# Kernel optimization log

Measured on AMD Instinct MI355X. Metric: run time of the kernel, lower is better.

The kernel has to match this reference:

```python
import jax, jax.numpy as jnp
import numpy as np

NUM_HEAVY = 1024
N_ITERS = 50
FETCH_K_RATIO = 9.0 / 8.0
EPS = 1.0


def rmsnorm(x, gamma):
    scale = gamma.shape[0] ** 0.5
    normed = x / jnp.maximum(jnp.linalg.norm(x, axis=-1, keepdims=True), 1e-12)
    return normed * scale * gamma


def feedforward(x, gamma, w1, b1, w2, b2):
    h = rmsnorm(x, gamma)
    h = jax.nn.gelu(h @ w1.T + b1, approximate=False)
    return h @ w2.T + b2


def coor_descent(s, n_iters, k, eps):
    # s: [b, n] router logits; faithful to lucidrains coor_descent (no mask, const eps)
    logk = jnp.log(jnp.asarray(k, s.dtype))
    a0 = jnp.zeros_like(s[..., :1])
    b0 = -s

    def body(carry, _):
        a, b = carry
        a = eps * (logk - jax.nn.logsumexp((s + b) / eps, axis=-1, keepdims=True))
        b = -jax.nn.relu(s + a)
        return (a, b), None

    (a, b), _ = jax.lax.scan(body, (a0, b0), None, length=n_iters)
    return jnp.exp((s + a + b) / eps)


def setup_inputs() -> dict:
    key = jax.random.key(0)
    ks = jax.random.split(key, 12)
    b, n, dim = 8, 8192, 1024
    d_light, d_heavy = int(dim * 0.5), dim * 4

    def lin(k, dout, din):
        bound = 1.0 / np.sqrt(din)
        k1, k2 = jax.random.split(k)
        w = jax.random.uniform(k1, (dout, din), jnp.float32, -bound, bound)
        bb = jax.random.uniform(k2, (dout,), jnp.float32, -bound, bound)
        return w, bb

    x = jax.random.normal(ks[0], (b, n, dim), jnp.float32)
    routing_token = jax.random.normal(ks[1], (dim,), jnp.float32)
    w1_l, b1_l = lin(ks[2], d_light, dim)
    w2_l, b2_l = lin(ks[3], dim, d_light)
    w1_h, b1_h = lin(ks[4], d_heavy, dim)
    w2_h, b2_h = lin(ks[5], dim, d_heavy)
    return dict(
        x=x, routing_token=routing_token,
        gamma_l=jnp.ones((dim,), jnp.float32), w1_l=w1_l, b1_l=b1_l, w2_l=w2_l, b2_l=b2_l,
        gamma_h=jnp.ones((dim,), jnp.float32), w1_h=w1_h, b1_h=b1_h, w2_h=w2_h, b2_h=b2_h,
    )


def reference(x, routing_token, gamma_l, w1_l, b1_l, w2_l, b2_l,
              gamma_h, w1_h, b1_h, w2_h, b2_h):
    b, n, dim = x.shape
    # light branch on all tokens
    light_out = feedforward(x, gamma_l, w1_l, b1_l, w2_l, b2_l)

    # router (coor_descent, num_routing_tokens=1, no mask)
    s = jnp.einsum('bnd,d->bn', x, routing_token)
    effective_k = min(NUM_HEAVY * FETCH_K_RATIO, n)
    scores = coor_descent(s, N_ITERS, effective_k, EPS)
    selected_scores, selected_indices = jax.lax.top_k(scores, NUM_HEAVY)
    # straight-through: value -> 1, grad flows through selected_scores
    selected_scores = selected_scores + jax.lax.stop_gradient(1.0 - selected_scores)

    # gather -> heavy FFN -> scale -> scatter back
    routed = jnp.take_along_axis(x, selected_indices[..., None], axis=1)  # [b, k, d]
    routed_out = feedforward(routed, gamma_h, w1_h, b1_h, w2_h, b2_h)
    routed_out = routed_out * selected_scores[..., None]

    batch_range = jnp.arange(b)[:, None]
    heavy_out = jnp.zeros_like(x).at[batch_range, selected_indices].set(routed_out)
    return light_out + heavy_out
```

## Files before the change

kernel.cpp:

```cpp
#include <hip/hip_runtime.h>
#include <cstdint>
#include <cstddef>


#define DEV __device__ __forceinline__

typedef __bf16 bf16x8 __attribute__((ext_vector_type(8)));
typedef float floatx4 __attribute__((ext_vector_type(4)));

DEV unsigned short f2bf(float f) {
  unsigned int u = __float_as_uint(f);
  u += 0x7FFFu + ((u >> 16) & 1u);
  return (unsigned short)(u >> 16);
}

__global__ __launch_bounds__(256) void convw_gamma_kernel(
    const float* __restrict__ w, const float* __restrict__ gamma,
    unsigned short* __restrict__ wb, int n) {
  int i = blockIdx.x * 256 + threadIdx.x;
  if (i < n) wb[i] = f2bf(w[i] * gamma[i & 1023]);
}
__global__ __launch_bounds__(256) void convw_kernel(
    const float* __restrict__ w, unsigned short* __restrict__ wb, int n) {
  int i = blockIdx.x * 256 + threadIdx.x;
  if (i < n) wb[i] = f2bf(w[i]);
}

__global__ __launch_bounds__(256) void prep_kernel(
    const float* __restrict__ x, const float* __restrict__ rt,
    unsigned short* __restrict__ xn, double* __restrict__ s) {
  const int token = blockIdx.x;
  const int tid = threadIdx.x;
  const float4 v = ((const float4*)(x + (size_t)token * 1024))[tid];
  const float4 r = ((const float4*)rt)[tid];
  float ss = v.x * v.x + v.y * v.y + v.z * v.z + v.w * v.w;
  double dot = (double)v.x * r.x + (double)v.y * r.y + (double)v.z * r.z + (double)v.w * r.w;
  const int wave = tid >> 6, lane = tid & 63;
#pragma unroll
  for (int off = 32; off; off >>= 1) {
    ss += __shfl_down(ss, off);
    dot += __shfl_down(dot, off);
  }
  __shared__ float ssr[4];
  __shared__ double dr[4];
  __shared__ float scale_sh;
  if (lane == 0) { ssr[wave] = ss; dr[wave] = dot; }
  __syncthreads();
  if (tid == 0) {
    float tot = ssr[0] + ssr[1] + ssr[2] + ssr[3];
    scale_sh = 32.0f / fmaxf(sqrtf(tot), 1e-12f);
    s[token] = dr[0] + dr[1] + dr[2] + dr[3];
  }
  __syncthreads();
  const float sc = scale_sh;
  ushort4 o;
  o.x = f2bf(v.x * sc); o.y = f2bf(v.y * sc);
  o.z = f2bf(v.z * sc); o.w = f2bf(v.w * sc);
  ((ushort4*)(xn + (size_t)token * 1024))[tid] = o;
}

__global__ __launch_bounds__(1024) void coor_kernel(
    const double* __restrict__ s, double* __restrict__ a_out) {
  const int b = blockIdx.x, tid = threadIdx.x;
  const int wave = tid >> 6, lane = tid & 63;
  __shared__ double red[16];
  __shared__ double bcast;
  const double* sb = s + (size_t)b * 8192;
  double sv[8], es[8];
#pragma unroll
  for (int i = 0; i < 8; ++i) {
    sv[i] = sb[tid * 8 + i];
    es[i] = exp(sv[i]);
  }
  const double logk = log(1152.0);
  double a = logk - log(8192.0);
  for (int it = 0; it < 49; ++it) {
    const double th = -a;
    const double eth = exp(th);
    double sum = 0.0;
#pragma unroll
    for (int i = 0; i < 8; ++i) sum += (sv[i] < th) ? es[i] : eth;
#pragma unroll
    for (int off = 32; off; off >>= 1) sum += __shfl_down(sum, off);
    if (lane == 0) red[wave] = sum;
    __syncthreads();
    if (tid == 0) {
      double t = 0.0;
      for (int i = 0; i < 16; ++i) t += red[i];
      bcast = logk - log(t);
    }
    __syncthreads();
    a = bcast;
  }
  if (tid == 0) a_out[b] = a;
}

__global__ __launch_bounds__(1024) void select_kernel(
    const double* __restrict__ s, const double* __restrict__ a_in,
    int* __restrict__ sel) {
  const int b = blockIdx.x, tid = threadIdx.x;
  const int wave = tid >> 6, lane = tid & 63;
  const double a = a_in[b];
  const double* sb = s + (size_t)b * 8192;
  const int base = tid * 8;
  double sv[8];
  bool ind[8];
  int cnt = 0;
#pragma unroll
  for (int i = 0; i < 8; ++i) {
    sv[i] = sb[base + i];
    ind[i] = (sv[i] + a >= 0.0);
    cnt += ind[i] ? 1 : 0;
  }
  __shared__ int sc[1024];
  sc[tid] = cnt;
  __syncthreads();
  for (int off = 1; off < 1024; off <<= 1) {
    int v = sc[tid];
    int add = (tid >= off) ? sc[tid - off] : 0;
    __syncthreads();
    sc[tid] = v + add;
    __syncthreads();
  }
  const int m = sc[1023];
  int p = sc[tid] - cnt;
#pragma unroll
  for (int i = 0; i < 8; ++i) {
    if (ind[i]) {
      if (p < 1024) sel[b * 1024 + p] = base + i;
      ++p;
    }
  }
  if (m >= 1024) return;

  __shared__ double rv[16];
  __shared__ int ri[16];
  __shared__ int gsel;
  bool taken[8] = {false, false, false, false, false, false, false, false};
  const int need = 1024 - m;
  for (int t = 0; t < need; ++t) {
    double bvv = -1.0e300;
    int bi = 0x7FFFFFFF;
#pragma unroll
    for (int i = 0; i < 8; ++i)
      if (!ind[i] && !taken[i] && sv[i] > bvv) { bvv = sv[i]; bi = base + i; }
#pragma unroll
    for (int off = 32; off; off >>= 1) {
      double ov = __shfl_down(bvv, off);
      int oi = __shfl_down(bi, off);
      if (ov > bvv || (ov == bvv && oi < bi)) { bvv = ov; bi = oi; }
    }
    if (lane == 0) { rv[wave] = bvv; ri[wave] = bi; }
    __syncthreads();
    if (tid == 0) {
      double mv = rv[0]; int mi = ri[0];
      for (int i = 1; i < 16; ++i)
        if (rv[i] > mv || (rv[i] == mv && ri[i] < mi)) { mv = rv[i]; mi = ri[i]; }
      gsel = mi;
      sel[b * 1024 + m + t] = mi;
    }
    __syncthreads();
    const int g = gsel;
    if (g >= base && g < base + 8) taken[g - base] = true;
    __syncthreads();
  }
}

__global__ __launch_bounds__(256) void gather_kernel(
    const unsigned short* __restrict__ xn, const int* __restrict__ sel,
    unsigned short* __restrict__ xg) {
  const int r = blockIdx.x;
  const int b = r >> 10;
  const int idx = sel[r];
  const uint2* src = (const uint2*)(xn + ((size_t)(b << 13) + idx) * 1024);
  uint2* dst = (uint2*)(xg + (size_t)r * 1024);
  dst[threadIdx.x] = src[threadIdx.x];
}

template <int MODE>
__global__ __launch_bounds__(256, 3) void gemm_bt_kernel(
    const unsigned short* __restrict__ A, const unsigned short* __restrict__ B,
    const float* __restrict__ bias, float* __restrict__ outF,
    unsigned short* __restrict__ outH, const int* __restrict__ sel,
    int M, int N, int K) {
  constexpr int BK = 32;
  __shared__ alignas(16) unsigned short As[128 * BK];
  __shared__ alignas(16) unsigned short Bs[128 * BK];
  const int tiles_n = N >> 7;
  const int bm = blockIdx.x / tiles_n;
  const int bn = blockIdx.x - bm * tiles_n;
  const int tid = threadIdx.x;
  const int wave = tid >> 6, lane = tid & 63;
  const int quad = lane >> 4, l16 = lane & 15;
  const int wm = (wave >> 1) << 6;
  const int wn = (wave & 1) << 6;

  floatx4 acc[4][4];
#pragma unroll
  for (int i = 0; i < 4; ++i)
#pragma unroll
    for (int j = 0; j < 4; ++j) acc[i][j] = 0.0f;

  const int sr = tid >> 2;
  const int scol = (tid & 3) << 3;
  const unsigned short* Ag = A + ((size_t)(bm * 128 + sr)) * K + scol;
  const unsigned short* Bg = B + ((size_t)(bn * 128 + sr)) * K + scol;
  const size_t rowstep = (size_t)64 * K;
  char* AsB = (char*)&As[0];
  char* BsB = (char*)&Bs[0];
  const int ldsbase = wave * 1024;

  for (int k0 = 0; k0 < K; k0 += BK) {
#pragma unroll
    for (int iss = 0; iss < 2; ++iss) {
      __builtin_amdgcn_global_load_lds(
          (__attribute__((address_space(1))) void*)(Ag + iss * rowstep + k0),
          (__attribute__((address_space(3))) void*)(AsB + ldsbase + iss * 4096), 16, 0, 0);
      __builtin_amdgcn_global_load_lds(
          (__attribute__((address_space(1))) void*)(Bg + iss * rowstep + k0),
          (__attribute__((address_space(3))) void*)(BsB + ldsbase + iss * 4096), 16, 0, 0);
    }
    __syncthreads();
    bf16x8 af[4], bfr[4];
#pragma unroll
    for (int mi = 0; mi < 4; ++mi)
      af[mi] = *(const bf16x8*)(As + (wm + mi * 16 + l16) * BK + quad * 8);
#pragma unroll
    for (int ni = 0; ni < 4; ++ni)
      bfr[ni] = *(const bf16x8*)(Bs + (wn + ni * 16 + l16) * BK + quad * 8);
#pragma unroll
    for (int mi = 0; mi < 4; ++mi)
#pragma unroll
      for (int ni = 0; ni < 4; ++ni)
        acc[mi][ni] = __builtin_amdgcn_mfma_f32_16x16x32_bf16(af[mi], bfr[ni], acc[mi][ni], 0, 0, 0);
    __syncthreads();
  }

  const int gm0 = bm * 128 + wm + quad * 4;
  const int gn0 = bn * 128 + wn + l16;
#pragma unroll
  for (int mi = 0; mi < 4; ++mi) {
#pragma unroll
    for (int ni = 0; ni < 4; ++ni) {
      const int col = gn0 + ni * 16;
      const float bv = bias[col];
#pragma unroll
      for (int r = 0; r < 4; ++r) {
        const int row = gm0 + mi * 16 + r;
        float v = acc[mi][ni][r] + bv;
        if (MODE == 0) {
          float g = 0.5f * v * (1.0f + erff(v * 0.70710678118654752f));
          outH[(size_t)row * N + col] = f2bf(g);
        } else if (MODE == 1) {
          outF[(size_t)row * N + col] = v;
        } else {
          const int idx = sel[row];
          const size_t op = (((size_t)((row >> 10) << 13) + idx) << 10) + col;
          outF[op] += v;
        }
      }
    }
  }
}

extern "C" void kernel_launch(void* const* d_in, const int* in_sizes, int n_in,
                              void* d_out, int out_size, void* d_ws, size_t ws_size,
                              hipStream_t stream) {
  const float* x    = (const float*)d_in[0];
  const float* rt   = (const float*)d_in[1];
  const float* g_l  = (const float*)d_in[2];
  const float* w1_l = (const float*)d_in[3];
  const float* b1_l = (const float*)d_in[4];
  const float* w2_l = (const float*)d_in[5];
  const float* b2_l = (const float*)d_in[6];
  const float* g_h  = (const float*)d_in[7];
  const float* w1_h = (const float*)d_in[8];
  const float* b1_h = (const float*)d_in[9];
  const float* w2_h = (const float*)d_in[10];
  const float* b2_h = (const float*)d_in[11];
  float* out = (float*)d_out;

  char* ws = (char*)d_ws;
  size_t off = 0;
  auto alloc = [&](size_t bytes) -> char* {
    char* p = ws + off;
    off += (bytes + 255) & ~(size_t)255;
    return p;
  };
  unsigned short* xn  = (unsigned short*)alloc((size_t)65536 * 1024 * 2);
  double* s           = (double*)alloc((size_t)65536 * 8);
  double* a_out       = (double*)alloc(256);
  int* sel            = (int*)alloc(8192 * 4);
  unsigned short* w1l = (unsigned short*)alloc((size_t)512 * 1024 * 2);
  unsigned short* w2l = (unsigned short*)alloc((size_t)1024 * 512 * 2);
  unsigned short* w1h = (unsigned short*)alloc((size_t)4096 * 1024 * 2);
  unsigned short* w2h = (unsigned short*)alloc((size_t)1024 * 4096 * 2);
  unsigned short* xg  = (unsigned short*)alloc((size_t)8192 * 1024 * 2);
  unsigned short* h1  = (unsigned short*)alloc((size_t)33554432 * 2);
  if (off > ws_size) return;

  convw_gamma_kernel<<<524288 / 256, 256, 0, stream>>>(w1_l, g_l, w1l, 524288);
  convw_kernel<<<524288 / 256, 256, 0, stream>>>(w2_l, w2l, 524288);
  convw_gamma_kernel<<<4194304 / 256, 256, 0, stream>>>(w1_h, g_h, w1h, 4194304);
  convw_kernel<<<4194304 / 256, 256, 0, stream>>>(w2_h, w2h, 4194304);

  prep_kernel<<<65536, 256, 0, stream>>>(x, rt, xn, s);
  coor_kernel<<<8, 1024, 0, stream>>>(s, a_out);
  select_kernel<<<8, 1024, 0, stream>>>(s, a_out, sel);
  gather_kernel<<<8192, 256, 0, stream>>>(xn, sel, xg);

  gemm_bt_kernel<0><<<512 * 4, 256, 0, stream>>>(xn, w1l, b1_l, nullptr, h1, nullptr, 65536, 512, 1024);
  gemm_bt_kernel<1><<<512 * 8, 256, 0, stream>>>(h1, w2l, b2_l, out, nullptr, nullptr, 65536, 1024, 512);
  gemm_bt_kernel<0><<<64 * 32, 256, 0, stream>>>(xg, w1h, b1_h, nullptr, h1, nullptr, 8192, 4096, 1024);
  gemm_bt_kernel<2><<<64 * 8, 256, 0, stream>>>(h1, w2h, b2_h, out, nullptr, sel, 8192, 1024, 4096);
}
```

Measured before the change: 1.020 ms.

## Add 256x256 multi-stage direct-to-LDS MFMA GEMM with XCD-aware tile swizzle

Introduces a new 512-thread GEMM kernel that computes 256x256 output tiles. It streams A and B tiles straight from global memory into LDS with global_load_lds, using a four-slot ring buffer, XOR-swizzled LDS addressing, vmcnt-based waits and s_setprio around the MFMA bursts. The goal is to overlap memory traffic with matrix math and raise data reuse per tile. The light up/down projections and the heavy up-projection now use this kernel, and a block-ID remap spreads neighbouring tiles across XCDs, also added to the old kernel still used for the heavy down-projection. The trade-off is 128KB of LDS per block, which caps occupancy, plus a larger accumulator register footprint.

Measured after the change: 951.6 us. 6.7% less time.

```diff
diff --git a/kernel.cpp b/kernel.cpp
--- a/kernel.cpp
+++ b/kernel.cpp
@@ -177,6 +177,167 @@
   dst[threadIdx.x] = src[threadIdx.x];
 }
 
+
+enum {
+  RA00 = 0,      RA01 = 16384,  RA10 = 32768,  RA11 = 49152,
+  RB00 = 65536,  RB01 = 81920,  RB10 = 98304,  RB11 = 114688
+};
+
+#define VMCNT(n) asm volatile("s_waitcnt vmcnt(" #n ")" ::: "memory")
+#define BARR() __builtin_amdgcn_s_barrier()
+#define SCHED0() __builtin_amdgcn_sched_barrier(0)
+
+#define STG_A(DST, KOFF)                                                      \
+  do {                                                                        \
+    _Pragma("unroll") for (int r_ = 0; r_ < 2; ++r_)                          \
+        __builtin_amdgcn_global_load_lds(                                     \
+            (__attribute__((address_space(1))) void*)(Asrc[r_] + (KOFF)),     \
+            (__attribute__((address_space(3))) void*)(sh + (DST) + r_ * 8192 +\
+                                                     ldsW),                   \
+            16, 0, 0);                                                        \
+  } while (0)
+
+#define STG_B(DST, KOFF)                                                      \
+  do {                                                                        \
+    _Pragma("unroll") for (int r_ = 0; r_ < 2; ++r_)                          \
+        __builtin_amdgcn_global_load_lds(                                     \
+            (__attribute__((address_space(1))) void*)(Bsrc[r_] + (KOFF)),     \
+            (__attribute__((address_space(3))) void*)(sh + (DST) + r_ * 8192 +\
+                                                     ldsW),                   \
+            16, 0, 0);                                                        \
+  } while (0)
+
+#define PH(RAOFF, RBOFF, MH, LOADB, STG)                                      \
+  do {                                                                        \
+    bf16x8 a_[4];                                                             \
+    _Pragma("unroll") for (int f_ = 0; f_ < 4; ++f_) a_[f_] =                 \
+        *(const bf16x8*)(sh + (RAOFF) + f_ * 2048 + rbA);                     \
+    if (LOADB) {                                                              \
+      _Pragma("unroll") for (int n_ = 0; n_ < 4; ++n_) bq[n_] =               \
+          *(const bf16x8*)(sh + (RBOFF) + n_ * 2048 + rbB);                   \
+    }                                                                         \
+    STG;                                                                      \
+    __builtin_amdgcn_s_setprio(1);                                            \
+    _Pragma("unroll") for (int f_ = 0; f_ < 4; ++f_)                          \
+        _Pragma("unroll") for (int n_ = 0; n_ < 4; ++n_) acc[(MH) + f_][n_] = \
+            __builtin_amdgcn_mfma_f32_16x16x32_bf16(a_[f_], bq[n_],           \
+                                                    acc[(MH) + f_][n_], 0, 0, \
+                                                    0);                       \
+    __builtin_amdgcn_s_setprio(0);                                            \
+  } while (0)
+
+#define ITER_FULL(I)                                                          \
+  do {                                                                        \
+    const int ks4 = ((2 * (I) + 1) << 6) + 32;                                \
+    const int ks1 = ((2 * (I) + 2) << 6);                                     \
+    const int ks2 = ks1 + 32;                                                 \
+    const int ks3 = ((2 * (I) + 3) << 6);                                     \
+    PH(RA00, RB00, 0, 1, STG_A(RA11, ks4));                                   \
+    PH(RA00 + 8192, RB00, 4, 0, STG_B(RB11, ks4));                            \
+    VMCNT(8); BARR(); SCHED0();                                               \
+    PH(RA01, RB01, 0, 1, STG_A(RA00, ks1));                                   \
+    PH(RA01 + 8192, RB01, 4, 0, STG_B(RB00, ks1));                            \
+    VMCNT(8); BARR(); SCHED0();                                               \
+    PH(RA10, RB10, 0, 1, STG_A(RA01, ks2));                                   \
+    PH(RA10 + 8192, RB10, 4, 0, STG_B(RB01, ks2));                            \
+    VMCNT(8); BARR(); SCHED0();                                               \
+    PH(RA11, RB11, 0, 1, STG_A(RA10, ks3));                                   \
+    PH(RA11 + 8192, RB11, 4, 0, STG_B(RB10, ks3));                            \
+    VMCNT(8); BARR(); SCHED0();                                               \
+  } while (0)
+
+#define ITER_LAST(I)                                                          \
+  do {                                                                        \
+    const int ks4 = ((2 * (I) + 1) << 6) + 32;                                \
+    PH(RA00, RB00, 0, 1, STG_A(RA11, ks4));                                   \
+    PH(RA00 + 8192, RB00, 4, 0, STG_B(RB11, ks4));                            \
+    VMCNT(8); BARR(); SCHED0();                                               \
+    PH(RA01, RB01, 0, 1, );                                                   \
+    PH(RA01 + 8192, RB01, 4, 0, );                                            \
+    VMCNT(4); BARR(); SCHED0();                                               \
+    PH(RA10, RB10, 0, 1, );                                                   \
+    PH(RA10 + 8192, RB10, 4, 0, );                                            \
+    VMCNT(0); BARR(); SCHED0();                                               \
+    PH(RA11, RB11, 0, 1, );                                                   \
+    PH(RA11 + 8192, RB11, 4, 0, );                                            \
+  } while (0)
+
+template <int MODE>
+__global__ __launch_bounds__(512, 2) void gemm8p_kernel(
+    const unsigned short* __restrict__ A, const unsigned short* __restrict__ B,
+    const float* __restrict__ bias, float* __restrict__ outF,
+    unsigned short* __restrict__ outH, int M, int N, int K) {
+  __shared__ alignas(16) char sh[131072];
+
+  const int tiles_n = N >> 8;
+  const int nwg = gridDim.x;
+  const int bid = blockIdx.x;
+  const int cpx = nwg >> 3;
+  const int swz = (bid & 7) * cpx + (bid >> 3);
+  const int bm = swz / tiles_n, bn = swz - bm * tiles_n;
+
+  const int tid = threadIdx.x;
+  const int wave = tid >> 6, lane = tid & 63;
+  const int l16 = lane & 15, q = lane >> 4;
+  const int wm = wave >> 2, wn = wave & 3;
+
+  const int slA = (((wm * 4 + q) ^ (l16 & 7)) << 4);
+  const int slB = ((((wn >> 1) * 4 + q) ^ (l16 & 7)) << 4);
+  const int rbA = l16 * 128 + slA;
+  const int rbB = (wn & 1) * 8192 + l16 * 128 + slB;
+
+  const int ssrc = (tid & 7) ^ ((tid >> 3) & 7);
+  const int hfold = ssrc >> 2, chunk = ssrc & 3;
+  const unsigned short* Asrc[2];
+  const unsigned short* Bsrc[2];
+#pragma unroll
+  for (int r = 0; r < 2; ++r) {
+    const int grow = r * 64 + (tid >> 3) + hfold * 128;
+    Asrc[r] = A + (size_t)(bm * 256 + grow) * K + chunk * 8;
+    Bsrc[r] = B + (size_t)(bn * 256 + grow) * K + chunk * 8;
+  }
+  const int ldsW = wave * 1024;
+
+  floatx4 acc[8][4];
+#pragma unroll
+  for (int i = 0; i < 8; ++i)
+#pragma unroll
+    for (int j = 0; j < 4; ++j) acc[i][j] = 0.0f;
+  bf16x8 bq[4];
+
+  STG_A(RA00, 0);  STG_B(RB00, 0);
+  STG_A(RA01, 32); STG_B(RB01, 32);
+  STG_A(RA10, 64); STG_B(RB10, 64);
+  VMCNT(8); BARR(); SCHED0();
+
+  const int NI = K >> 7;
+#pragma unroll 1
+  for (int i = 0; i < NI - 1; ++i) ITER_FULL(i);
+  ITER_LAST(NI - 1);
+
+  const int gm0 = bm * 256 + wm * 128 + q * 4;
+  const int gn0 = bn * 256 + wn * 64 + l16;
+#pragma unroll
+  for (int m = 0; m < 8; ++m) {
+#pragma unroll
+    for (int n = 0; n < 4; ++n) {
+      const int col = gn0 + n * 16;
+      const float bv = bias[col];
+#pragma unroll
+      for (int r = 0; r < 4; ++r) {
+        const int row = gm0 + m * 16 + r;
+        float v = acc[m][n][r] + bv;
+        if (MODE == 0) {
+          float g = 0.5f * v * (1.0f + erff(v * 0.70710678118654752f));
+          outH[(size_t)row * N + col] = f2bf(g);
+        } else {
+          outF[(size_t)row * N + col] = v;
+        }
+      }
+    }
+  }
+}
+
 template <int MODE>
 __global__ __launch_bounds__(256, 3) void gemm_bt_kernel(
     const unsigned short* __restrict__ A, const unsigned short* __restrict__ B,
@@ -187,8 +348,12 @@
   __shared__ alignas(16) unsigned short As[128 * BK];
   __shared__ alignas(16) unsigned short Bs[128 * BK];
   const int tiles_n = N >> 7;
-  const int bm = blockIdx.x / tiles_n;
-  const int bn = blockIdx.x - bm * tiles_n;
+  int bid = blockIdx.x;
+  if ((gridDim.x & 7) == 0) {
+    bid = (bid & 7) * (gridDim.x >> 3) + (bid >> 3);
+  }
+  const int bm = bid / tiles_n;
+  const int bn = bid - bm * tiles_n;
   const int tid = threadIdx.x;
   const int wave = tid >> 6, lane = tid & 63;
   const int quad = lane >> 4, l16 = lane & 15;
@@ -309,8 +474,8 @@
   select_kernel<<<8, 1024, 0, stream>>>(s, a_out, sel);
   gather_kernel<<<8192, 256, 0, stream>>>(xn, sel, xg);
 
-  gemm_bt_kernel<0><<<512 * 4, 256, 0, stream>>>(xn, w1l, b1_l, nullptr, h1, nullptr, 65536, 512, 1024);
-  gemm_bt_kernel<1><<<512 * 8, 256, 0, stream>>>(h1, w2l, b2_l, out, nullptr, nullptr, 65536, 1024, 512);
-  gemm_bt_kernel<0><<<64 * 32, 256, 0, stream>>>(xg, w1h, b1_h, nullptr, h1, nullptr, 8192, 4096, 1024);
+  gemm8p_kernel<0><<<256 * 2, 512, 0, stream>>>(xn, w1l, b1_l, nullptr, h1, 65536, 512, 1024);
+  gemm8p_kernel<1><<<256 * 4, 512, 0, stream>>>(h1, w2l, b2_l, out, nullptr, 65536, 1024, 512);
+  gemm8p_kernel<0><<<32 * 16, 512, 0, stream>>>(xg, w1h, b1_h, nullptr, h1, 8192, 4096, 1024);
   gemm_bt_kernel<2><<<64 * 8, 256, 0, stream>>>(h1, w2h, b2_h, out, nullptr, sel, 8192, 1024, 4096);
 }
```
